# Kernel optimization log

Hardware: AMD Instinct MI355X
Metric: run time of the kernel (lower is better)

## Reference

```python
import jax, jax.numpy as jnp
import numpy as np

EPS = 1e-4
HEADS = 16
DH = 64


def setup_inputs() -> dict:
    key = jax.random.key(0)
    ks = jax.random.split(key, 5)
    b, t, d = 2, 2048, 1024
    return {
        "X": jax.random.normal(ks[0], (b, t, d), dtype=jnp.float32),
        "W_in": jax.random.normal(ks[1], (HEADS * 4 * DH, d), dtype=jnp.float32) * (1.0 / np.sqrt(d)),
        "b_in": jax.random.normal(ks[2], (HEADS * 4 * DH,), dtype=jnp.float32) * 0.01,
        "W_out": jax.random.normal(ks[3], (d, HEADS * DH), dtype=jnp.float32) * (1.0 / np.sqrt(HEADS * DH)),
        "b_out": jax.random.normal(ks[4], (d,), dtype=jnp.float32) * 0.01,
    }


def reference(X, W_in, b_in, W_out, b_out):
    b, t, d = X.shape
    # project_in: [b,t,h*4*dh] -> [b,t,h,4*dh] -> [b,h,t,4*dh]
    P = jnp.einsum('btd,ed->bte', X, W_in) + b_in
    P = P.reshape(b, t, HEADS, 4 * DH).transpose(0, 2, 1, 3)
    Q, K, V, G = jnp.split(P, 4, axis=-1)  # each [b,h,t,dh]
    # Euclidean cdist: sqrt(||q||^2 + ||k||^2 - 2 q.k), clamped at 0
    q2 = jnp.sum(Q * Q, axis=-1)[..., :, None]   # [b,h,t,1]
    k2 = jnp.sum(K * K, axis=-1)[..., None, :]   # [b,h,1,t]
    qk = jnp.einsum('bhqd,bhkd->bhqk', Q, K)
    dist = jnp.sqrt(jnp.maximum(q2 + k2 - 2.0 * qk, 0.0))
    # Shepard weights: (eps + dist)^-2, normalized over keys
    W = (EPS + dist) ** (-2)
    W = W / (EPS + jnp.sum(W, axis=-1, keepdims=True))
    A = jnp.einsum('bhqk,bhkd->bhqd', W, V)
    # gate, merge heads: [b,h,t,dh] -> [b,t,h*dh]
    H = (G * A).transpose(0, 2, 1, 3).reshape(b, t, HEADS * DH)
    Y = jnp.einsum('bte,de->btd', H, W_out) + b_out
    return Y
```

## Files before the change

### kernel.cpp

```cpp
#include <hip/hip_runtime.h>
#include <math.h>

#define EPS 1e-4f


typedef __attribute__((ext_vector_type(8))) short bf16x8;
typedef __attribute__((ext_vector_type(8))) unsigned short u16x8;
typedef __attribute__((ext_vector_type(4))) float f32x4;

#define MFMA(a, b, c) __builtin_amdgcn_mfma_f32_16x16x32_bf16(a, b, c, 0, 0, 0)

__device__ __forceinline__ unsigned short f2b(float f) {
    unsigned int u = __float_as_uint(f);
    u += 0x7fffu + ((u >> 16) & 1u);
    return (unsigned short)(u >> 16);
}
__device__ __forceinline__ float b2f(unsigned short u) {
    return __uint_as_float(((unsigned int)u) << 16);
}
__device__ __forceinline__ unsigned int cvtpk(float a, float b) {
    unsigned int r;
    asm("v_cvt_pk_bf16_f32 %0, %1, %2" : "=v"(r) : "v"(a), "v"(b));
    return r;
}

typedef __attribute__((address_space(1))) const unsigned int as1_u32;
typedef __attribute__((address_space(3))) unsigned int as3_u32;
__device__ __forceinline__ void gl_lds16(const unsigned short* g, unsigned short* l) {
    __builtin_amdgcn_global_load_lds((as1_u32*)g, (as3_u32*)l, 16, 0, 0);
}

__global__ __launch_bounds__(256)
void sga_f2b(const float* __restrict__ src, unsigned short* __restrict__ dst, int n8) {
    int i = blockIdx.x * 256 + threadIdx.x;
    const int stride = gridDim.x * 256;
    for (; i < n8; i += stride) {
        const float4* s = (const float4*)src + i * 2;
        float4 a = s[0], b = s[1];
        uint4 o;
        o.x = (unsigned)f2b(a.x) | ((unsigned)f2b(a.y) << 16);
        o.y = (unsigned)f2b(a.z) | ((unsigned)f2b(a.w) << 16);
        o.z = (unsigned)f2b(b.x) | ((unsigned)f2b(b.y) << 16);
        o.w = (unsigned)f2b(b.z) | ((unsigned)f2b(b.w) << 16);
        *((uint4*)dst + i) = o;
    }
}

__global__ __launch_bounds__(256)
void sga_gemm1(const unsigned short* __restrict__ Xb, const unsigned short* __restrict__ Wb,
               const float* __restrict__ bin,
               unsigned short* __restrict__ Qb, unsigned short* __restrict__ Kb,
               unsigned short* __restrict__ Vt, unsigned short* __restrict__ Gb,
               float* __restrict__ q2s, float* __restrict__ k2s)
{
    __shared__ unsigned short As[128 * 64];
    __shared__ unsigned short Bs[128 * 64];
    const int tid = threadIdx.x;
    const int lane = tid & 63, w = tid >> 6;
    const int lr = lane & 15, lg = lane >> 4;
    const int wm = w & 1, wn = w >> 1;
    const int m0 = blockIdx.y * 128, n0 = blockIdx.x * 128;

    const int sr = tid >> 3, sc8 = tid & 7;
    const int gch = sc8 ^ (sr & 7);
    const unsigned short* aBase = Xb + (m0 + sr) * 1024 + gch * 8;
    const unsigned short* bBase = Wb + (n0 + sr) * 1024 + gch * 8;
    unsigned short* aDst = &As[w * 512];
    unsigned short* bDst = &Bs[w * 512];

    f32x4 acc[4][4] = {};

    for (int kt = 0; kt < 16; ++kt) {
        __syncthreads();
        #pragma unroll
        for (int c = 0; c < 4; ++c)
            gl_lds16(aBase + c * 32768 + kt * 64, aDst + c * 2048);
        #pragma unroll
        for (int c = 0; c < 4; ++c)
            gl_lds16(bBase + c * 32768 + kt * 64, bDst + c * 2048);
        __syncthreads();

        #pragma unroll
        for (int ks = 0; ks < 2; ++ks) {
            bf16x8 af[4], bfr[4];
            #pragma unroll
            for (int i = 0; i < 4; ++i) {
                const int row = wm * 64 + i * 16 + lr;
                af[i] = *(const bf16x8*)&As[row * 64 + (((ks * 4 + lg) ^ (row & 7)) * 8)];
            }
            #pragma unroll
            for (int i = 0; i < 4; ++i) {
                const int row = wn * 64 + i * 16 + lr;
                bfr[i] = *(const bf16x8*)&Bs[row * 64 + (((ks * 4 + lg) ^ (row & 7)) * 8)];
            }
            #pragma unroll
            for (int mi = 0; mi < 4; ++mi)
                #pragma unroll
                for (int ni = 0; ni < 4; ++ni)
                    acc[mi][ni] = MFMA(af[mi], bfr[ni], acc[mi][ni]);
        }
    }

    const int bb = m0 >> 11;
    const bool qkBlock = ((n0 & 128) == 0);
    #pragma unroll
    for (int mf = 0; mf < 4; ++mf) {
        const int tbase = m0 + wm * 64 + mf * 16 + lg * 4;
        const int tloc = tbase & 2047;
        float s2[4] = {0.f, 0.f, 0.f, 0.f};
        #pragma unroll
        for (int nf = 0; nf < 4; ++nf) {
            const int n = n0 + wn * 64 + nf * 16 + lr;
            const int h = n >> 8, cc = n & 255;
            const int part = cc >> 6, j = cc & 63;
            const int bh = bb * 16 + h;
            const float bz = bin[n];
            f32x4 v = acc[mf][nf];
            unsigned short e0 = f2b(v[0] + bz), e1 = f2b(v[1] + bz),
                           e2 = f2b(v[2] + bz), e3 = f2b(v[3] + bz);
            if (qkBlock) {
                float f0 = b2f(e0), f1 = b2f(e1), f2 = b2f(e2), f3 = b2f(e3);
                s2[0] += f0 * f0; s2[1] += f1 * f1;
                s2[2] += f2 * f2; s2[3] += f3 * f3;
            }
            if (part == 2) {
                ushort4 pk = make_ushort4(e0, e1, e2, e3);
                *(ushort4*)&Vt[(bh * 64 + j) * 2048 + tloc] = pk;
            } else {
                unsigned short* dst = (part == 0) ? Qb : ((part == 1) ? Kb : Gb);
                unsigned short vv[4] = {e0, e1, e2, e3};
                #pragma unroll
                for (int r = 0; r < 4; ++r)
                    dst[(bh * 2048 + tloc + r) * 64 + j] = vv[r];
            }
        }
        if (qkBlock) {
            const int bh = bb * 16 + (n0 >> 8);
            float* __restrict__ dstn = wn ? k2s : q2s;
            #pragma unroll
            for (int r = 0; r < 4; ++r) {
                float v = s2[r];
                v += __shfl_xor(v, 1, 64); v += __shfl_xor(v, 2, 64);
                v += __shfl_xor(v, 4, 64); v += __shfl_xor(v, 8, 64);
                if (lr == 0) dstn[bh * 2048 + ((tloc + r) & 2047)] = v;
            }
        }
    }
}

__global__ __launch_bounds__(256, 4)
void sga_attn(const unsigned short* __restrict__ Qb, const unsigned short* __restrict__ Kb,
              const unsigned short* __restrict__ Vt,
              const float* __restrict__ q2s, const float* __restrict__ k2s,
              unsigned short* __restrict__ Op0, unsigned short* __restrict__ Op1,
              unsigned short* __restrict__ Op2, unsigned short* __restrict__ Op3,
              float* __restrict__ Sw0, float* __restrict__ Sw1,
              float* __restrict__ Sw2, float* __restrict__ Sw3)
{
    __shared__ unsigned short Klds[2 * 4096];
    __shared__ unsigned short Vlds[2 * 4096];
    __shared__ unsigned short Wlds[4 * 2048];

    const int tid = threadIdx.x;
    const int lane = tid & 63, w = tid >> 6;
    const int lr = lane & 15, lg = lane >> 4;

    const int qt = blockIdx.x, bh = blockIdx.y, half = blockIdx.z;
    const int q0 = qt * 128 + w * 32;
    const int kbeg = half * 8, kend = kbeg + 8;

    unsigned short* wl = &Wlds[w * 2048];
    unsigned short* __restrict__ Op =
        (half & 2) ? ((half & 1) ? Op3 : Op2) : ((half & 1) ? Op1 : Op0);
    float* __restrict__ Sw =
        (half & 2) ? ((half & 1) ? Sw3 : Sw2) : ((half & 1) ? Sw1 : Sw0);

    const int sr8 = tid >> 3, sch = tid & 7;
    const int gch = sch ^ (sr8 & 7);
    const unsigned short* Kg = Kb + bh * 2048 * 64;
    const unsigned short* Vg = Vt + bh * 64 * 2048;
    unsigned short* kDst = &Klds[w * 512];
    unsigned short* vDst = &Vlds[w * 512];

    bf16x8 qf[2][2];
    #pragma unroll
    for (int g = 0; g < 2; ++g) {
        const unsigned short* qp = Qb + (bh * 2048 + q0 + g * 16 + lr) * 64 + lg * 8;
        qf[g][0] = *(const bf16x8*)qp;
        qf[g][1] = *(const bf16x8*)(qp + 32);
    }
    float q2v[2];
    q2v[0] = q2s[bh * 2048 + q0 + lr];
    q2v[1] = q2s[bh * 2048 + q0 + 16 + lr];

    f32x4 oacc[2][4] = {};
    float sumw[2] = {0.f, 0.f};

    #pragma unroll
    for (int c = 0; c < 2; ++c) {
        const int row = c * 32 + sr8;
        gl_lds16(Kg + (kbeg * 64 + row) * 64 + gch * 8, kDst + c * 2048);
        gl_lds16(Vg + row * 2048 + kbeg * 64 + gch * 8, vDst + c * 2048);
    }
    __syncthreads();

    int buf = 0;
    for (int kt = kbeg; kt < kend; ++kt) {
        const int k0 = kt * 64;
        const bool more = (kt + 1 < kend);

        if (more) {
            const int bo = (buf ^ 1) * 4096;
            #pragma unroll
            for (int c = 0; c < 2; ++c) {
                const int row = c * 32 + sr8;
                gl_lds16(Kg + ((k0 + 64) + row) * 64 + gch * 8, kDst + bo + c * 2048);
                gl_lds16(Vg + row * 2048 + (k0 + 64) + gch * 8, vDst + bo + c * 2048);
            }
        }

        const unsigned short* kb = &Klds[buf * 4096];
        const unsigned short* vb = &Vlds[buf * 4096];

        f32x4 k2v[4];
        #pragma unroll
        for (int nf = 0; nf < 4; ++nf)
            k2v[nf] = *(const f32x4*)&k2s[bh * 2048 + k0 + nf * 16 + lg * 4];

        f32x4 sa[2][4] = {};
        __builtin_amdgcn_s_setprio(1);
        #pragma unroll
        for (int nf = 0; nf < 4; ++nf) {
            const int row = nf * 16 + lr;
            bf16x8 kf0 = *(const bf16x8*)&kb[row * 64 + ((lg ^ (row & 7)) * 8)];
            bf16x8 kf1 = *(const bf16x8*)&kb[row * 64 + (((4 + lg) ^ (row & 7)) * 8)];
            #pragma unroll
            for (int g = 0; g < 2; ++g) {
                sa[g][nf] = MFMA(kf0, qf[g][0], sa[g][nf]);
                sa[g][nf] = MFMA(kf1, qf[g][1], sa[g][nf]);
            }
        }
        __builtin_amdgcn_s_setprio(0);

        #pragma unroll
        for (int g = 0; g < 2; ++g) {
            const int row = g * 16 + lr;
            #pragma unroll
            for (int nf = 0; nf < 4; ++nf) {
                float wv[4];
                #pragma unroll
                for (int r = 0; r < 4; ++r) {
                    float d2 = fmaf(-2.0f, sa[g][nf][r], q2v[g] + k2v[nf][r]);
                    d2 = fmaxf(d2, 1e-8f);
                    wv[r] = __builtin_amdgcn_rcpf(d2);
                    sumw[g] += wv[r];
                }
                uint2 pk;
                pk.x = cvtpk(wv[0], wv[1]);
                pk.y = cvtpk(wv[2], wv[3]);
                const int c = 2 * nf + (lg >> 1);
                *(uint2*)&wl[row * 64 + ((c ^ (row & 7)) * 8) + (lg & 1) * 4] = pk;
            }
        }

        bf16x8 pa[2][2];
        #pragma unroll
        for (int g = 0; g < 2; ++g) {
            const int row = g * 16 + lr;
            pa[g][0] = *(const bf16x8*)&wl[row * 64 + ((lg ^ (row & 7)) * 8)];
            pa[g][1] = *(const bf16x8*)&wl[row * 64 + (((4 + lg) ^ (row & 7)) * 8)];
        }
        __builtin_amdgcn_s_setprio(1);
        #pragma unroll
        for (int vf = 0; vf < 4; ++vf) {
            const int row = vf * 16 + lr;
            bf16x8 v0 = *(const bf16x8*)&vb[row * 64 + ((lg ^ (row & 7)) * 8)];
            bf16x8 v1 = *(const bf16x8*)&vb[row * 64 + (((4 + lg) ^ (row & 7)) * 8)];
            #pragma unroll
            for (int g = 0; g < 2; ++g) {
                oacc[g][vf] = MFMA(pa[g][0], v0, oacc[g][vf]);
                oacc[g][vf] = MFMA(pa[g][1], v1, oacc[g][vf]);
            }
        }
        __builtin_amdgcn_s_setprio(0);

        if (more) {
            __syncthreads();
            buf ^= 1;
        }
    }

    #pragma unroll
    for (int g = 0; g < 2; ++g) {
        sumw[g] += __shfl_xor(sumw[g], 16, 64);
        sumw[g] += __shfl_xor(sumw[g], 32, 64);
    }

    #pragma unroll
    for (int g = 0; g < 2; ++g) {
        #pragma unroll
        for (int vf = 0; vf < 4; ++vf) {
            #pragma unroll
            for (int r = 0; r < 4; ++r) {
                const int t = q0 + g * 16 + lg * 4 + r;
                const int dh = vf * 16 + lr;
                Op[(bh * 2048 + t) * 64 + dh] = f2b(oacc[g][vf][r]);
            }
        }
    }
    if (lg == 0) {
        Sw[bh * 2048 + q0 + lr]      = sumw[0];
        Sw[bh * 2048 + q0 + 16 + lr] = sumw[1];
    }
}

__global__ __launch_bounds__(256)
void sga_combine(const unsigned short* __restrict__ Op0, const unsigned short* __restrict__ Op1,
                 const unsigned short* __restrict__ Op2, const unsigned short* __restrict__ Op3,
                 const float* __restrict__ Sw0, const float* __restrict__ Sw1,
                 const float* __restrict__ Sw2, const float* __restrict__ Sw3,
                 const unsigned short* __restrict__ Gb, unsigned short* __restrict__ Hb)
{
    const int idx = blockIdx.x * 256 + threadIdx.x;
    const int t16 = idx >> 3;
    const int dq = (idx & 7) << 3;
    u16x8 a = *(const u16x8*)&Op0[t16 * 64 + dq];
    u16x8 b = *(const u16x8*)&Op1[t16 * 64 + dq];
    u16x8 c = *(const u16x8*)&Op2[t16 * 64 + dq];
    u16x8 d = *(const u16x8*)&Op3[t16 * 64 + dq];
    u16x8 g = *(const u16x8*)&Gb[t16 * 64 + dq];
    const float s = Sw0[t16] + Sw1[t16] + Sw2[t16] + Sw3[t16];
    const float inv = __builtin_amdgcn_rcpf(EPS + s);
    const int bh = t16 >> 11, tloc = t16 & 2047;
    const int bb = bh >> 4, h = bh & 15;
    u16x8 o;
    #pragma unroll
    for (int j = 0; j < 8; ++j)
        o[j] = f2b((b2f(a[j]) + b2f(b[j]) + b2f(c[j]) + b2f(d[j])) * inv * b2f(g[j]));
    *(u16x8*)&Hb[(bb * 2048 + tloc) * 1024 + h * 64 + dq] = o;
}

__global__ __launch_bounds__(256)
void sga_gemm2(const unsigned short* __restrict__ Hb, const unsigned short* __restrict__ Wb,
               const float* __restrict__ bout, float* __restrict__ Y)
{
    __shared__ unsigned short As[128 * 64];
    __shared__ unsigned short Bs[128 * 64];
    const int tid = threadIdx.x;
    const int lane = tid & 63, w = tid >> 6;
    const int lr = lane & 15, lg = lane >> 4;
    const int wm = w & 1, wn = w >> 1;
    const int m0 = blockIdx.y * 128, n0 = blockIdx.x * 128;

    const int sr = tid >> 3, sc8 = tid & 7;
    const int gch = sc8 ^ (sr & 7);
    const unsigned short* aBase = Hb + (m0 + sr) * 1024 + gch * 8;
    const unsigned short* bBase = Wb + (n0 + sr) * 1024 + gch * 8;
    unsigned short* aDst = &As[w * 512];
    unsigned short* bDst = &Bs[w * 512];

    f32x4 acc[4][4] = {};

    for (int kt = 0; kt < 16; ++kt) {
        __syncthreads();
        #pragma unroll
        for (int c = 0; c < 4; ++c)
            gl_lds16(aBase + c * 32768 + kt * 64, aDst + c * 2048);
        #pragma unroll
        for (int c = 0; c < 4; ++c)
            gl_lds16(bBase + c * 32768 + kt * 64, bDst + c * 2048);
        __syncthreads();

        #pragma unroll
        for (int ks = 0; ks < 2; ++ks) {
            bf16x8 af[4], bfr[4];
            #pragma unroll
            for (int i = 0; i < 4; ++i) {
                const int row = wm * 64 + i * 16 + lr;
                af[i] = *(const bf16x8*)&As[row * 64 + (((ks * 4 + lg) ^ (row & 7)) * 8)];
            }
            #pragma unroll
            for (int i = 0; i < 4; ++i) {
                const int row = wn * 64 + i * 16 + lr;
                bfr[i] = *(const bf16x8*)&Bs[row * 64 + (((ks * 4 + lg) ^ (row & 7)) * 8)];
            }
            #pragma unroll
            for (int mi = 0; mi < 4; ++mi)
                #pragma unroll
                for (int ni = 0; ni < 4; ++ni)
                    acc[mi][ni] = MFMA(af[mi], bfr[ni], acc[mi][ni]);
        }
    }

    #pragma unroll
    for (int mf = 0; mf < 4; ++mf) {
        const int m = m0 + wm * 64 + mf * 16 + lg * 4;
        #pragma unroll
        for (int nf = 0; nf < 4; ++nf) {
            const int n = n0 + wn * 64 + nf * 16 + lr;
            const float bz = bout[n];
            f32x4 v = acc[mf][nf];
            #pragma unroll
            for (int r = 0; r < 4; ++r)
                Y[(m + r) * 1024 + n] = v[r] + bz;
        }
    }
}

extern "C" void kernel_launch(void* const* d_in, const int* in_sizes, int n_in,
                              void* d_out, int out_size, void* d_ws, size_t ws_size,
                              hipStream_t stream) {
    const float* X    = (const float*)d_in[0];
    const float* Win  = (const float*)d_in[1];
    const float* bin  = (const float*)d_in[2];
    const float* Wout = (const float*)d_in[3];
    const float* bout = (const float*)d_in[4];
    float* Y = (float*)d_out;

    const int PER = 32 * 2048 * 64;
    unsigned short* Qb   = (unsigned short*)d_ws;
    unsigned short* Kb   = Qb + PER;
    unsigned short* Vt   = Kb + PER;
    unsigned short* Gb   = Vt + PER;
    unsigned short* Hb   = Gb + PER;
    unsigned short* Xb   = Hb + PER;
    unsigned short* Winb = Xb + PER;
    unsigned short* Woutb= Winb + PER;
    float* q2s = (float*)(Woutb + 1024 * 1024);
    float* k2s = q2s + 32 * 2048;
    float* Sw0 = k2s + 32 * 2048;
    float* Sw1 = Sw0 + 32 * 2048;
    float* Sw2 = Sw1 + 32 * 2048;
    float* Sw3 = Sw2 + 32 * 2048;
    unsigned short* Op2 = (unsigned short*)(Sw3 + 32 * 2048);
    unsigned short* Op3 = Op2 + PER;
    unsigned short* Op0 = Xb;
    unsigned short* Op1 = Winb;

    sga_f2b<<<1024, 256, 0, stream>>>(X, Xb, 524288);
    sga_f2b<<<1024, 256, 0, stream>>>(Win, Winb, 524288);
    sga_f2b<<<256, 256, 0, stream>>>(Wout, Woutb, 131072);
    sga_gemm1<<<dim3(32, 32), 256, 0, stream>>>(Xb, Winb, bin, Qb, Kb, Vt, Gb, q2s, k2s);
    sga_attn <<<dim3(16, 32, 4), 256, 0, stream>>>(Qb, Kb, Vt, q2s, k2s,
                                                   Op0, Op1, Op2, Op3, Sw0, Sw1, Sw2, Sw3);
    sga_combine<<<2048, 256, 0, stream>>>(Op0, Op1, Op2, Op3, Sw0, Sw1, Sw2, Sw3, Gb, Hb);
    sga_gemm2<<<dim3(8, 32), 256, 0, stream>>>(Hb, Woutb, bout, Y);
}
```

Before: 163.6 us.

## Fuse fp32-to-bf16 casts and enlarge attention blocks with XCD-aware tile mapping

Merges the three conversion launches into one kernel that dispatches on thread index. The attention kernel now runs 512-thread blocks covering 256 queries, so each K/V tile staged in LDS serves twice as many query rows. Block IDs are remapped so that work sharing a head and key range lands on the same XCD for L2 locality. K/V staging switches from direct global-to-LDS loads to register-staged loads written to LDS after the compute phase, which costs registers and may limit occupancy at 512 threads.

After: 161.4 us. Within noise of the previous version (-1.3%).

```diff
diff --git a/kernel.cpp b/kernel.cpp
--- a/kernel.cpp
+++ b/kernel.cpp
@@ -31,19 +31,23 @@
 }
 
 __global__ __launch_bounds__(256)
-void sga_f2b(const float* __restrict__ src, unsigned short* __restrict__ dst, int n8) {
-    int i = blockIdx.x * 256 + threadIdx.x;
-    const int stride = gridDim.x * 256;
-    for (; i < n8; i += stride) {
-        const float4* s = (const float4*)src + i * 2;
-        float4 a = s[0], b = s[1];
-        uint4 o;
-        o.x = (unsigned)f2b(a.x) | ((unsigned)f2b(a.y) << 16);
-        o.y = (unsigned)f2b(a.z) | ((unsigned)f2b(a.w) << 16);
-        o.z = (unsigned)f2b(b.x) | ((unsigned)f2b(b.y) << 16);
-        o.w = (unsigned)f2b(b.z) | ((unsigned)f2b(b.w) << 16);
-        *((uint4*)dst + i) = o;
-    }
+void sga_f2b_all(const float* __restrict__ X, const float* __restrict__ Win,
+                 const float* __restrict__ Wout,
+                 unsigned short* __restrict__ Xb, unsigned short* __restrict__ Winb,
+                 unsigned short* __restrict__ Woutb) {
+    const int i = blockIdx.x * 256 + threadIdx.x;
+    const float* src; unsigned short* dst; int off;
+    if (i < 524288)        { src = X;    dst = Xb;    off = i; }
+    else if (i < 1048576)  { src = Win;  dst = Winb;  off = i - 524288; }
+    else                   { src = Wout; dst = Woutb; off = i - 1048576; }
+    const float4* s = (const float4*)src + off * 2;
+    float4 a = s[0], b = s[1];
+    uint4 o;
+    o.x = (unsigned)f2b(a.x) | ((unsigned)f2b(a.y) << 16);
+    o.y = (unsigned)f2b(a.z) | ((unsigned)f2b(a.w) << 16);
+    o.z = (unsigned)f2b(b.x) | ((unsigned)f2b(b.y) << 16);
+    o.w = (unsigned)f2b(b.z) | ((unsigned)f2b(b.w) << 16);
+    *((uint4*)dst + off) = o;
 }
 
 __global__ __launch_bounds__(256)
@@ -148,7 +152,7 @@
     }
 }
 
-__global__ __launch_bounds__(256, 4)
+__global__ __launch_bounds__(512, 4)
 void sga_attn(const unsigned short* __restrict__ Qb, const unsigned short* __restrict__ Kb,
               const unsigned short* __restrict__ Vt,
               const float* __restrict__ q2s, const float* __restrict__ k2s,
@@ -159,14 +163,18 @@
 {
     __shared__ unsigned short Klds[2 * 4096];
     __shared__ unsigned short Vlds[2 * 4096];
-    __shared__ unsigned short Wlds[4 * 2048];
+    __shared__ unsigned short Wlds[8 * 2048];
 
     const int tid = threadIdx.x;
     const int lane = tid & 63, w = tid >> 6;
     const int lr = lane & 15, lg = lane >> 4;
 
-    const int qt = blockIdx.x, bh = blockIdx.y, half = blockIdx.z;
-    const int q0 = qt * 128 + w * 32;
+    const int lin = blockIdx.x;
+    const int xcd = lin & 7, rem = lin >> 3;
+    const int gid = xcd * 16 + (rem >> 3);
+    const int qt = rem & 7;
+    const int half = gid >> 5, bh = gid & 31;
+    const int q0 = qt * 256 + w * 32;
     const int kbeg = half * 8, kend = kbeg + 8;
 
     unsigned short* wl = &Wlds[w * 2048];
@@ -175,12 +183,10 @@
     float* __restrict__ Sw =
         (half & 2) ? ((half & 1) ? Sw3 : Sw2) : ((half & 1) ? Sw1 : Sw0);
 
-    const int sr8 = tid >> 3, sch = tid & 7;
-    const int gch = sch ^ (sr8 & 7);
-    const unsigned short* Kg = Kb + bh * 2048 * 64;
-    const unsigned short* Vg = Vt + bh * 64 * 2048;
-    unsigned short* kDst = &Klds[w * 512];
-    unsigned short* vDst = &Vlds[w * 512];
+    const int srow = tid >> 3, sch = tid & 7;
+    const unsigned short* Kg = Kb + (bh * 2048 + srow) * 64 + sch * 8;
+    const unsigned short* Vg = Vt + (bh * 64 + srow) * 2048 + sch * 8;
+    const int swz = srow * 64 + ((sch ^ (srow & 7)) * 8);
 
     bf16x8 qf[2][2];
     #pragma unroll
@@ -196,12 +202,10 @@
     f32x4 oacc[2][4] = {};
     float sumw[2] = {0.f, 0.f};
 
-    #pragma unroll
-    for (int c = 0; c < 2; ++c) {
-        const int row = c * 32 + sr8;
-        gl_lds16(Kg + (kbeg * 64 + row) * 64 + gch * 8, kDst + c * 2048);
-        gl_lds16(Vg + row * 2048 + kbeg * 64 + gch * 8, vDst + c * 2048);
-    }
+    uint4 ks = *(const uint4*)(Kg + kbeg * 4096);
+    uint4 vs = *(const uint4*)(Vg + kbeg * 64);
+    *(uint4*)&Klds[swz] = ks;
+    *(uint4*)&Vlds[swz] = vs;
     __syncthreads();
 
     int buf = 0;
@@ -210,17 +214,9 @@
         const bool more = (kt + 1 < kend);
 
         if (more) {
-            const int bo = (buf ^ 1) * 4096;
-            #pragma unroll
-            for (int c = 0; c < 2; ++c) {
-                const int row = c * 32 + sr8;
-                gl_lds16(Kg + ((k0 + 64) + row) * 64 + gch * 8, kDst + bo + c * 2048);
-                gl_lds16(Vg + row * 2048 + (k0 + 64) + gch * 8, vDst + bo + c * 2048);
-            }
-        }
-
-        const unsigned short* kb = &Klds[buf * 4096];
-        const unsigned short* vb = &Vlds[buf * 4096];
+            ks = *(const uint4*)(Kg + (kt + 1) * 4096);
+            vs = *(const uint4*)(Vg + (kt + 1) * 64);
+        }
 
         f32x4 k2v[4];
         #pragma unroll
@@ -228,6 +224,7 @@
             k2v[nf] = *(const f32x4*)&k2s[bh * 2048 + k0 + nf * 16 + lg * 4];
 
         f32x4 sa[2][4] = {};
+        const unsigned short* kb = &Klds[buf * 4096];
         __builtin_amdgcn_s_setprio(1);
         #pragma unroll
         for (int nf = 0; nf < 4; ++nf) {
@@ -270,6 +267,7 @@
             pa[g][0] = *(const bf16x8*)&wl[row * 64 + ((lg ^ (row & 7)) * 8)];
             pa[g][1] = *(const bf16x8*)&wl[row * 64 + (((4 + lg) ^ (row & 7)) * 8)];
         }
+        const unsigned short* vb = &Vlds[buf * 4096];
         __builtin_amdgcn_s_setprio(1);
         #pragma unroll
         for (int vf = 0; vf < 4; ++vf) {
@@ -285,6 +283,9 @@
         __builtin_amdgcn_s_setprio(0);
 
         if (more) {
+            const int bo = (buf ^ 1) * 4096;
+            *(uint4*)&Klds[bo + swz] = ks;
+            *(uint4*)&Vlds[bo + swz] = vs;
             __syncthreads();
             buf ^= 1;
         }
@@ -437,12 +438,10 @@
     unsigned short* Op0 = Xb;
     unsigned short* Op1 = Winb;
 
-    sga_f2b<<<1024, 256, 0, stream>>>(X, Xb, 524288);
-    sga_f2b<<<1024, 256, 0, stream>>>(Win, Winb, 524288);
-    sga_f2b<<<256, 256, 0, stream>>>(Wout, Woutb, 131072);
+    sga_f2b_all<<<4608, 256, 0, stream>>>(X, Win, Wout, Xb, Winb, Woutb);
     sga_gemm1<<<dim3(32, 32), 256, 0, stream>>>(Xb, Winb, bin, Qb, Kb, Vt, Gb, q2s, k2s);
-    sga_attn <<<dim3(16, 32, 4), 256, 0, stream>>>(Qb, Kb, Vt, q2s, k2s,
-                                                   Op0, Op1, Op2, Op3, Sw0, Sw1, Sw2, Sw3);
+    sga_attn <<<1024, 512, 0, stream>>>(Qb, Kb, Vt, q2s, k2s,
+                                        Op0, Op1, Op2, Op3, Sw0, Sw1, Sw2, Sw3);
     sga_combine<<<2048, 256, 0, stream>>>(Op0, Op1, Op2, Op3, Sw0, Sw1, Sw2, Sw3, Gb, Hb);
     sga_gemm2<<<dim3(8, 32), 256, 0, stream>>>(Hb, Woutb, bout, Y);
 }
```
